# Performance work log

Hardware: AMD Instinct MI355X
Metric: run time of the kernel (lower is better)

Reference implementation:

```python
import jax, jax.numpy as jnp
import numpy as np

PAD_TOKEN = 1
V_EN = 32000
V_DE = 32000
WORD_DIM = 300
HID = 500
VLAYER = 500


def lstm(x, Wih, Whh, bih, bhh):
    """Single-layer batch-first LSTM, PyTorch gate order (i,f,g,o). x: [B,T,D] -> h: [B,T,H]."""
    xg = jnp.einsum('btd,gd->btg', x, Wih) + bih  # precompute input projections [B,T,4H]
    H = Whh.shape[1]
    B = x.shape[0]

    def step(carry, xg_t):
        h, c = carry
        g = xg_t + h @ Whh.T + bhh
        i, f, gg, o = jnp.split(g, 4, axis=-1)
        c = jax.nn.sigmoid(f) * c + jax.nn.sigmoid(i) * jnp.tanh(gg)
        h = jax.nn.sigmoid(o) * jnp.tanh(c)
        return (h, c), h

    h0 = jnp.zeros((B, H), x.dtype)
    (_, _), hs = jax.lax.scan(step, (h0, h0), jnp.swapaxes(xg, 0, 1))
    return jnp.swapaxes(hs, 0, 1)


def setup_inputs() -> dict:
    key = jax.random.key(0)
    ks = jax.random.split(key, 12)
    B, S, T = 64, 50, 50
    s = 0.05
    inp = {
        'x_de': jax.random.randint(ks[0], (B, S), 0, V_DE),
        'x_en': jax.random.randint(ks[1], (B, T), 0, V_EN),
        'emb_de_w': jax.random.normal(ks[2], (V_DE, WORD_DIM)) * s,
        'emb_en_w': jax.random.normal(ks[3], (V_EN, WORD_DIM)) * s,
        'enc_Wih': jax.random.normal(ks[4], (4 * HID, WORD_DIM)) * s,
        'enc_Whh': jax.random.normal(ks[5], (4 * HID, HID)) * s,
        'enc_bih': jnp.zeros((4 * HID,)),
        'enc_bhh': jnp.zeros((4 * HID,)),
        'dec_Wih': jax.random.normal(ks[6], (4 * HID, WORD_DIM)) * s,
        'dec_Whh': jax.random.normal(ks[7], (4 * HID, HID)) * s,
        'dec_bih': jnp.zeros((4 * HID,)),
        'dec_bhh': jnp.zeros((4 * HID,)),
        'h2e_w': jax.random.normal(ks[8], (VLAYER, 2 * HID)) * s,
        'h2e_b': jnp.zeros((VLAYER,)),
        'e2v_w': jax.random.normal(ks[9], (V_EN, VLAYER)) * s,
        'e2v_b': jnp.zeros((V_EN,)),
    }
    return inp


def reference(x_de, x_en, emb_de_w, emb_en_w,
              enc_Wih, enc_Whh, enc_bih, enc_bhh,
              dec_Wih, dec_Whh, dec_bih, dec_bhh,
              h2e_w, h2e_b, e2v_w, e2v_b):
    emb_de = emb_de_w[x_de]                       # [B,S,D]
    emb_en = emb_en_w[x_en]                       # [B,T,D]
    enc_h = lstm(emb_de, enc_Wih, enc_Whh, enc_bih, enc_bhh)  # [B,S,H]
    dec_h = lstm(emb_en, dec_Wih, dec_Whh, dec_bih, dec_bhh)  # [B,T,H]

    Tm1 = dec_h.shape[1] - 1
    scores = jnp.einsum('bsh,bth->bst', enc_h, dec_h[:, :Tm1])  # [B,S,T']

    # hard attention: categorical sample per (b,t), all timesteps vectorized
    logp_attn = jax.nn.log_softmax(scores, axis=1)               # [B,S,T']
    samples = jax.random.categorical(jax.random.key(42),
                                     jnp.swapaxes(scores, 1, 2), axis=-1)  # [B,T'] int
    context = jnp.take_along_axis(enc_h, samples[:, :, None], axis=1)      # [B,T',H]

    feat = jnp.concatenate([dec_h[:, :Tm1], context], axis=-1)   # [B,T',2H]
    e = jnp.tanh(feat @ h2e_w.T + h2e_b)
    pred = jax.nn.log_softmax(e @ e2v_w.T + e2v_b, axis=-1)      # [B,T',V]

    y = x_en[:, 1:]                                              # [B,T']
    mask = (y != PAD_TOKEN).astype(pred.dtype)
    reward = jnp.take_along_axis(pred, y[:, :, None], axis=-1)[..., 0]  # [B,T']
    cnt = jnp.maximum(mask.sum(0), 1.0)

    loss = -jnp.sum((reward * mask).sum(0) / cnt)

    logp_s = jnp.take_along_axis(jnp.swapaxes(logp_attn, 1, 2),
                                 samples[:, :, None], axis=-1)[..., 0]  # [B,T']
    baseline = jnp.log(1.0 / V_EN)
    adv = jax.lax.stop_gradient(reward - baseline)
    reinforce_loss = -jnp.sum((logp_s * adv * mask).sum(0) / cnt)

    return loss, reinforce_loss
```

## Files before the change

kernel.cpp:

```cpp
#include <hip/hip_runtime.h>
#include <cstdint>

typedef short short8 __attribute__((ext_vector_type(8)));
typedef float f32x4 __attribute__((ext_vector_type(4)));
typedef uint32_t u32x4 __attribute__((ext_vector_type(4)));
typedef unsigned short u16;
typedef unsigned long long u64;

__device__ __forceinline__ u16 f2bf(float f) {
  union { float f; uint32_t u; } v; v.f = f;
  uint32_t u = v.u;
  uint32_t r = (u + 0x7fffu + ((u >> 16) & 1u)) >> 16;
  return (u16)r;
}
__device__ __forceinline__ float bf2f(u16 b) {
  union { uint32_t u; float f; } v; v.u = ((uint32_t)b) << 16; return v.f;
}
__device__ __forceinline__ float sigm(float x) { return 1.f / (1.f + expf(-x)); }
__device__ __forceinline__ float tanh_f(float x) { return 2.f / (1.f + expf(-2.f * x)) - 1.f; }

typedef const __attribute__((address_space(1))) uint32_t glb_u32;
typedef __attribute__((address_space(3))) uint32_t lds_u32;
__device__ __forceinline__ void glds16(const void* g, void* l) {
  __builtin_amdgcn_global_load_lds((glb_u32*)g, (lds_u32*)l, 16, 0, 0);
}

__device__ __forceinline__ void tfround(uint32_t& a, uint32_t& b, int r) {
  a += b; b = (b << r) | (b >> (32 - r)); b ^= a;
}
__device__ __forceinline__ void threefry(uint32_t k0, uint32_t k1, uint32_t& x0, uint32_t& x1) {
  uint32_t k2 = k0 ^ k1 ^ 0x1BD11BDAu;
  x0 += k0; x1 += k1;
  tfround(x0,x1,13); tfround(x0,x1,15); tfround(x0,x1,26); tfround(x0,x1,6);
  x0 += k1; x1 += k2 + 1u;
  tfround(x0,x1,17); tfround(x0,x1,29); tfround(x0,x1,16); tfround(x0,x1,24);
  x0 += k2; x1 += k0 + 2u;
  tfround(x0,x1,13); tfround(x0,x1,15); tfround(x0,x1,26); tfround(x0,x1,6);
  x0 += k0; x1 += k1 + 3u;
  tfround(x0,x1,17); tfround(x0,x1,29); tfround(x0,x1,16); tfround(x0,x1,24);
  x0 += k1; x1 += k2 + 4u;
  tfround(x0,x1,13); tfround(x0,x1,15); tfround(x0,x1,26); tfround(x0,x1,6);
  x0 += k2; x1 += k0 + 5u;
}
__device__ __forceinline__ float gumbel_from_bits(uint32_t bits) {
  float f = __uint_as_float((bits >> 9) | 0x3f800000u) - 1.0f;
  const float tiny = 1.17549435e-38f;
  float u = fmaxf(f + tiny, tiny);
  return -logf(-logf(u));
}

__global__ __launch_bounds__(256) void prep_all(
    const float* eWih, const float* eWhh, const float* ebih, const float* ebhh,
    const float* dWih, const float* dWhh, const float* dbih, const float* dbhh,
    const float* h2e_w, const float* h2e_b, const float* e2v_w,
    u16* wih_p, u16* whh_p, float* bsum, u16* h2e_p, float* h2e_bp,
    u16* e2v_p, u16* hglob, int* bar)
{
  const uint32_t GWIH = 2u*2048u*40u;
  const uint32_t GWHH = 2u*2048u*64u;
  const uint32_t GBS  = 512u;
  const uint32_t GH2E = 512u*128u;
  const uint32_t GH2EB= 64u;
  const uint32_t GE2V = 32000u*64u;
  const uint32_t GHG  = 16384u;
  const uint32_t GBAR = 64u;
  const uint32_t TOT  = GWIH+GWHH+GBS+GH2E+GH2EB+GE2V+GHG+GBAR;
  for (uint32_t i = blockIdx.x*256u + threadIdx.x; i < TOT; i += gridDim.x*256u) {
    uint32_t j = i;
    if (j < GWIH) {
      uint32_t L = j / (2048u*40u), rem = j % (2048u*40u);
      uint32_t p = rem / 40u, kg = rem % 40u;
      uint32_t g = p >> 9, u = p & 511u, k0 = kg*8u;
      short8 o = {0,0,0,0,0,0,0,0}; u16* op = (u16*)&o;
      if (u < 500u) {
        const float* src = (L ? dWih : eWih) + ((size_t)(g*500u+u))*300u + k0;
        if (k0 + 8u <= 300u) {
          float4 a = *(const float4*)src, b = *(const float4*)(src+4);
          op[0]=f2bf(a.x);op[1]=f2bf(a.y);op[2]=f2bf(a.z);op[3]=f2bf(a.w);
          op[4]=f2bf(b.x);op[5]=f2bf(b.y);op[6]=f2bf(b.z);op[7]=f2bf(b.w);
        } else {
          #pragma unroll
          for (int e = 0; e < 8; ++e) if (k0+e < 300u) op[e] = f2bf(src[e]);
        }
      }
      *(short8*)(wih_p + (size_t)j*8) = o; continue;
    }
    j -= GWIH;
    if (j < GWHH) {
      uint32_t L = j / (2048u*64u), rem = j % (2048u*64u);
      uint32_t row = rem >> 6, kg = rem & 63u, k0 = kg*8u;
      uint32_t wg = row >> 7, r2 = row & 127u, g = r2 >> 5, ul = r2 & 31u;
      uint32_t u = wg*32u + ul;
      short8 o = {0,0,0,0,0,0,0,0}; u16* op = (u16*)&o;
      if (u < 500u) {
        const float* src = (L ? dWhh : eWhh) + ((size_t)(g*500u+u))*500u + k0;
        if (k0 + 8u <= 500u) {
          float4 a = *(const float4*)src, b = *(const float4*)(src+4);
          op[0]=f2bf(a.x);op[1]=f2bf(a.y);op[2]=f2bf(a.z);op[3]=f2bf(a.w);
          op[4]=f2bf(b.x);op[5]=f2bf(b.y);op[6]=f2bf(b.z);op[7]=f2bf(b.w);
        } else {
          #pragma unroll
          for (int e = 0; e < 8; ++e) if (k0+e < 500u) op[e] = f2bf(src[e]);
        }
      }
      *(short8*)(whh_p + (size_t)j*8) = o; continue;
    }
    j -= GWHH;
    if (j < GBS) {
      uint32_t L = j >> 8, pg = j & 255u, p0 = pg*8u;
      float arr[8];
      #pragma unroll
      for (int e = 0; e < 8; ++e) {
        uint32_t p = p0 + e, g = p >> 9, u = p & 511u;
        arr[e] = (u < 500u) ? ((L?dbih:ebih)[g*500u+u] + (L?dbhh:ebhh)[g*500u+u]) : 0.f;
      }
      *(float4*)(bsum + (size_t)j*8) = *(float4*)arr;
      *(float4*)(bsum + (size_t)j*8 + 4) = *(float4*)(arr+4);
      continue;
    }
    j -= GBS;
    if (j < GH2E) {
      uint32_t n = j >> 7, kg = j & 127u, k0 = kg*8u;
      short8 o = {0,0,0,0,0,0,0,0}; u16* op = (u16*)&o;
      if (n < 500u) {
        const float* rowp = h2e_w + (size_t)n*1000u;
        if (k0 + 8u <= 500u) {
          float4 a = *(const float4*)(rowp+k0), b = *(const float4*)(rowp+k0+4);
          op[0]=f2bf(a.x);op[1]=f2bf(a.y);op[2]=f2bf(a.z);op[3]=f2bf(a.w);
          op[4]=f2bf(b.x);op[5]=f2bf(b.y);op[6]=f2bf(b.z);op[7]=f2bf(b.w);
        } else if (k0 >= 512u && k0 + 8u <= 1012u) {
          #pragma unroll
          for (int e = 0; e < 8; ++e) op[e] = f2bf(rowp[k0 + e - 12u]);
        } else {
          #pragma unroll
          for (int e = 0; e < 8; ++e) {
            uint32_t k = k0 + e; float v = 0.f;
            if (k < 500u) v = rowp[k];
            else if (k >= 512u && k < 1012u) v = rowp[k - 12u];
            op[e] = f2bf(v);
          }
        }
      }
      *(short8*)(h2e_p + (size_t)j*8) = o; continue;
    }
    j -= GH2E;
    if (j < GH2EB) {
      uint32_t k0 = j*8u;
      float arr[8];
      #pragma unroll
      for (int e = 0; e < 8; ++e) { uint32_t k = k0+e; arr[e] = (k < 500u) ? h2e_b[k] : 0.f; }
      *(float4*)(h2e_bp + (size_t)j*8) = *(float4*)arr;
      *(float4*)(h2e_bp + (size_t)j*8 + 4) = *(float4*)(arr+4);
      continue;
    }
    j -= GH2EB;
    if (j < GE2V) {
      uint32_t n = j >> 6, kg = j & 63u, k0 = kg*8u;
      short8 o = {0,0,0,0,0,0,0,0}; u16* op = (u16*)&o;
      const float* src = e2v_w + (size_t)n*500u + k0;
      if (k0 + 8u <= 500u) {
        float4 a = *(const float4*)src, b = *(const float4*)(src+4);
        op[0]=f2bf(a.x);op[1]=f2bf(a.y);op[2]=f2bf(a.z);op[3]=f2bf(a.w);
        op[4]=f2bf(b.x);op[5]=f2bf(b.y);op[6]=f2bf(b.z);op[7]=f2bf(b.w);
      } else {
        #pragma unroll
        for (int e = 0; e < 8; ++e) if (k0+e < 500u) op[e] = f2bf(src[e]);
      }
      *(short8*)(e2v_p + (size_t)j*8) = o; continue;
    }
    j -= GE2V;
    if (j < GHG) { short8 z = {0,0,0,0,0,0,0,0}; *(short8*)(hglob + (size_t)j*8) = z; continue; }
    j -= GHG;
    if (j < GBAR) bar[j] = 0;
  }
}

__global__ __launch_bounds__(256, 1) void lstm_kernel(
    const u16* xg , const u16* whh_p,
    u16* hglob , float* h_out , int* bar)
{
  const int wg = blockIdx.x;
  const int lstm = wg >> 4;
  const int wgl = wg & 15;
  const int tid = threadIdx.x;
  const int wid = tid >> 6;
  const int lane = tid & 63;

  __shared__ u16 hbuf[64 * 512];
  __shared__ float pre[4][64][34];
  __shared__ u16 hsh[64 * 32];

  short8 wf[2][16];
  {
    const u16* wbase = whh_p + ((size_t)lstm*2048 + wgl*128 + wid*32) * 512;
    #pragma unroll
    for (int nt = 0; nt < 2; ++nt)
      #pragma unroll
      for (int kk = 0; kk < 16; ++kk) {
        int row = nt*16 + (lane & 15);
        int k = kk*32 + (lane >> 4)*8;
        wf[nt][kk] = *(const short8*)(wbase + (size_t)row*512 + k);
      }
  }

  float c[8];
  #pragma unroll
  for (int q = 0; q < 8; ++q) c[q] = 0.f;

  int* mybar = bar + lstm*32;
  const int ug = wgl*32 + (tid & 31);
  const u16* xgl = xg + ((size_t)lstm*3200)*2048;

  float xr[4][8];
  #pragma unroll
  for (int q = 0; q < 8; ++q) {
    int b = q*8 + (tid >> 5);
    size_t xrow = ((size_t)(b*50 + 0))*2048;
    #pragma unroll
    for (int g = 0; g < 4; ++g) xr[g][q] = bf2f(xgl[xrow + g*512 + ug]);
  }

  #pragma unroll 1
  for (int t = 0; t < 50; ++t) {
    const int cur = t & 1;
    {
      u32x4 sv[16];
      const char* sbase = (const char*)(hglob + ((size_t)(cur*2 + lstm))*64*512);
      #pragma unroll
      for (int i = 0; i < 16; ++i) {
        const void* p = sbase + (size_t)(i*256 + tid)*16;
        asm volatile("global_load_dwordx4 %0, %1, off sc0 sc1" : "=v"(sv[i]) : "v"(p));
      }
      asm volatile("s_waitcnt vmcnt(0)" ::: "memory");
      __builtin_amdgcn_sched_barrier(0);
      #pragma unroll
      for (int i = 0; i < 16; ++i) {
        int chunk = i*256 + tid;
        int row = chunk >> 6, col16 = chunk & 63;
        int byte = row*1024 + ((col16*16) ^ ((row & 7) << 4));
        *(u32x4*)((char*)hbuf + byte) = sv[i];
      }
    }
    __syncthreads();

    f32x4 zero = {0.f, 0.f, 0.f, 0.f};
    f32x4 acc[4][2];
    #pragma unroll
    for (int m = 0; m < 4; ++m) { acc[m][0] = zero; acc[m][1] = zero; }

    #pragma unroll
    for (int kk = 0; kk < 16; ++kk) {
      short8 af[4];
      #pragma unroll
      for (int m = 0; m < 4; ++m) {
        int row = m*16 + (lane & 15);
        int byte = row*1024 + ((kk*64 + (lane >> 4)*16) ^ ((row & 7) << 4));
        af[m] = *(const short8*)((const char*)hbuf + byte);
      }
      #pragma unroll
      for (int m = 0; m < 4; ++m) {
        acc[m][0] = __builtin_amdgcn_mfma_f32_16x16x32_bf16(af[m], wf[0][kk], acc[m][0], 0, 0, 0);
        acc[m][1] = __builtin_amdgcn_mfma_f32_16x16x32_bf16(af[m], wf[1][kk], acc[m][1], 0, 0, 0);
      }
    }

    #pragma unroll
    for (int m = 0; m < 4; ++m)
      #pragma unroll
      for (int nt = 0; nt < 2; ++nt)
        #pragma unroll
        for (int jj = 0; jj < 4; ++jj) {
          int row = m*16 + (lane >> 4)*4 + jj;
          int col = nt*16 + (lane & 15);
          pre[wid][row][col] = acc[m][nt][jj];
        }
    __syncthreads();

    #pragma unroll
    for (int q = 0; q < 8; ++q) {
      int b = q*8 + (tid >> 5);
      int ul = tid & 31;
      float pi = pre[0][b][ul] + xr[0][q];
      float pf = pre[1][b][ul] + xr[1][q];
      float pg = pre[2][b][ul] + xr[2][q];
      float po = pre[3][b][ul] + xr[3][q];
      c[q] = sigm(pf)*c[q] + sigm(pi)*tanh_f(pg);
      float h = sigm(po)*tanh_f(c[q]);
      if (ug >= 500) h = 0.f;
      h_out[(((size_t)(lstm*64 + b))*50 + t)*512 + ug] = h;
      hsh[b*32 + ul] = f2bf(h);
    }
    if (t == 49) break;
    __syncthreads();

    {
      u16* hdst = hglob + ((size_t)((cur^1)*2 + lstm))*64*512;
      int b2 = tid >> 2, c8 = (tid & 3)*8;
      u32x4 w = *(const u32x4*)(hsh + b2*32 + c8);
      void* dp = hdst + (size_t)b2*512 + wgl*32 + c8;
      asm volatile("global_store_dwordx4 %0, %1, off sc0 sc1" :: "v"(dp), "v"(w) : "memory");
    }
    asm volatile("s_waitcnt vmcnt(0)" ::: "memory");

    if (tid == 0)
      __hip_atomic_fetch_add(mybar, 1, __ATOMIC_RELAXED, __HIP_MEMORY_SCOPE_AGENT);

    {
      const int tn = t + 1;
      #pragma unroll
      for (int q = 0; q < 8; ++q) {
        int b = q*8 + (tid >> 5);
        size_t xrow = ((size_t)(b*50 + tn))*2048;
        #pragma unroll
        for (int g = 0; g < 4; ++g) xr[g][q] = bf2f(xgl[xrow + g*512 + ug]);
      }
    }

    if (tid == 0) {
      int target = 16*(t+1);
      while (__hip_atomic_load(mybar, __ATOMIC_RELAXED, __HIP_MEMORY_SCOPE_AGENT) < target) {}
    }
    __syncthreads();
  }
}

__global__ __launch_bounds__(256) void scores_kernel(const float* h_out, float* scores) {
  int b = blockIdx.x >> 2, tq = blockIdx.x & 3;
  int tid = threadIdx.x, wid = tid >> 6, lane = tid & 63;
  __shared__ float enc[50*512];
  const float* ebase = h_out + ((size_t)b*50)*512;
  for (int i = tid*4; i < 50*512; i += 256*4)
    *(float4*)(enc + i) = *(const float4*)(ebase + i);
  __syncthreads();
  const int t0 = tq*13;
  const int cnt = (tq == 3) ? 10 : 13;
  for (int tl = wid; tl < cnt; tl += 4) {
    int t = t0 + tl;
    const float* drow = h_out + ((size_t)((64 + b)*50 + t))*512;
    float d[8];
    #pragma unroll
    for (int j = 0; j < 8; ++j) d[j] = drow[lane + j*64];
    for (int s = 0; s < 50; ++s) {
      float p = 0.f;
      #pragma unroll
      for (int j = 0; j < 8; ++j) p += enc[s*512 + lane + j*64] * d[j];
      #pragma unroll
      for (int mk = 32; mk; mk >>= 1) p += __shfl_xor(p, mk);
      if (lane == 0) scores[((size_t)(b*50 + s))*49 + t] = p;
    }
  }
}

__global__ __launch_bounds__(256) void sample_kernel(const float* scores, int* samples, float* logp_s) {
  int p = blockIdx.x*4 + (threadIdx.x >> 6);
  int lane = threadIdx.x & 63;
  int b = p / 49, t = p - b*49;
  float sc = -INFINITY;
  if (lane < 50) sc = scores[((size_t)(b*50 + lane))*49 + t];
  float val = -INFINITY;
  if (lane < 50) {
    uint32_t i = (uint32_t)(p*50 + lane);
    uint32_t x0, x1; int sel;
    if (i < 78400u) { x0 = i; x1 = i + 78400u; sel = 0; }
    else            { x0 = i - 78400u; x1 = i; sel = 1; }
    threefry(0u, 42u, x0, x1);
    val = sc + gumbel_from_bits(sel ? x1 : x0);
  }
  int idx = lane; float v = val;
  #pragma unroll
  for (int mk = 1; mk < 64; mk <<= 1) {
    float ov = __shfl_xor(v, mk);
    int oi = __shfl_xor(idx, mk);
    if (ov > v || (ov == v && oi < idx)) { v = ov; idx = oi; }
  }
  float m = sc;
  #pragma unroll
  for (int mk = 1; mk < 64; mk <<= 1) m = fmaxf(m, __shfl_xor(m, mk));
  float e = (lane < 50) ? expf(sc - m) : 0.f;
  #pragma unroll
  for (int mk = 1; mk < 64; mk <<= 1) e += __shfl_xor(e, mk);
  float lse = m + logf(e);
  float scs = __shfl(sc, idx);
  if (lane == 0) { samples[p] = idx; logp_s[p] = scs - lse; }
}

template <int AMODE, int EPI>
__global__ __launch_bounds__(256) void gemm_k(
    const float* Af32a, const float* Af32b, const int* gia, const int* gib,
    const u16* Abf, const u16* Bp, int ldkB, int KT,
    float* Cf32, u16* Cbf, const float* bias,
    float* pm, float* ps, float* ylogit)
{
  int Mb, Nb;
  if constexpr (EPI == 2) {
    int bid = blockIdx.y*gridDim.x + blockIdx.x;
    const int NBLK = 25*250, q = NBLK/8, r = NBLK%8;
    int xcd = bid & 7, idx = bid >> 3;
    int wgid = (xcd < r ? xcd*(q+1) : r*(q+1) + (xcd-r)*q) + idx;
    Mb = wgid % 25; Nb = wgid / 25;
  } else { Mb = blockIdx.x; Nb = blockIdx.y; }
  const int zb = blockIdx.z;
  const int tid = threadIdx.x;
  const int wid = tid >> 6, lane = tid & 63;
  const int wr = wid >> 1, wc = wid & 1;

  __shared__ u16 As[2*128*64];
  __shared__ u16 Bs[2*128*64];
  __shared__ float part[128][2][2];

  f32x4 zero = {0.f,0.f,0.f,0.f};
  f32x4 acc[4][4];
  #pragma unroll
  for (int m = 0; m < 4; ++m)
    #pragma unroll
    for (int n = 0; n < 4; ++n) acc[m][n] = zero;

  auto MFMA_STEP = [&](int buf) {
    #pragma unroll
    for (int kk2 = 0; kk2 < 2; ++kk2) {
      short8 a[4], b[4];
      #pragma unroll
      for (int m = 0; m < 4; ++m) {
        int row = wr*64 + m*16 + (lane & 15);
        int byte = buf*16384 + row*128 + ((kk2*64 + (lane >> 4)*16) ^ ((row & 7) << 4));
        a[m] = *(const short8*)((const char*)As + byte);
      }
      #pragma unroll
      for (int n = 0; n < 4; ++n) {
        int row = wc*64 + n*16 + (lane & 15);
        int byte = buf*16384 + row*128 + ((kk2*64 + (lane >> 4)*16) ^ ((row & 7) << 4));
        b[n] = *(const short8*)((const char*)Bs + byte);
      }
      #pragma unroll
      for (int m = 0; m < 4; ++m)
        #pragma unroll
        for (int n = 0; n < 4; ++n)
          acc[m][n] = __builtin_amdgcn_mfma_f32_16x16x32_bf16(a[m], b[n], acc[m][n], 0, 0, 0);
    }
  };

  if constexpr (AMODE == 2) {
    auto ISSUE = [&](int it, int buf) {
      #pragma unroll
      for (int i = 0; i < 4; ++i) {
        int chunk = i*256 + tid;
        int row = chunk >> 3, c16 = chunk & 7;
        int cg = c16 ^ (row & 7);
        const u16* sa = Abf + (size_t)(Mb*128 + row)*512 + it*64 + cg*8;
        const u16* sb = Bp  + (size_t)(Nb*128 + row)*512 + it*64 + cg*8;
        char* da = (char*)As + buf*16384 + i*4096 + wid*1024;
        char* db = (char*)Bs + buf*16384 + i*4096 + wid*1024;
        glds16(sa, da);
        glds16(sb, db);
      }
    };
    ISSUE(0, 0);
    asm volatile("s_waitcnt vmcnt(0)" ::: "memory");
    __syncthreads();
    for (int it = 0; it < KT; ++it) {
      const int buf = it & 1;
      if (it + 1 < KT) ISSUE(it + 1, buf ^ 1);
      MFMA_STEP(buf);
      if (it + 1 < KT) {
        asm volatile("s_waitcnt vmcnt(0)" ::: "memory");
        __syncthreads();
      }
    }
  } else {
    const int r = tid >> 1;
    const int koff = (tid & 1)*32;
    const int growA = Mb*128 + r;
    const int growB = Nb*128 + r;

    const float* emb = nullptr; const int* ids = nullptr;
    int fb = 0, ft = 0, fsmp = 0; bool fvalid = true;
    if constexpr (AMODE == 0) {
      emb = zb ? Af32b : Af32a;
      ids = zb ? gib : gia;
    } else {
      fvalid = growA < 3136;
      fb = growA / 49; ft = growA - fb*49;
      fsmp = fvalid ? gia[growA] : 0;
    }

    short8 av8[4], bv8[4];
    auto FETCH = [&](int it) {
      const int k0 = it*64 + koff;
      u16* avp = (u16*)av8;
      if constexpr (AMODE == 0) {
        const float* srow = emb + (size_t)ids[growA]*300;
        #pragma unroll
        for (int j = 0; j < 8; ++j) {
          int k = k0 + j*4;
          float4 v = make_float4(0.f,0.f,0.f,0.f);
          if (k + 4 <= 300) v = *(const float4*)(srow + k);
          avp[j*4+0]=f2bf(v.x); avp[j*4+1]=f2bf(v.y); avp[j*4+2]=f2bf(v.z); avp[j*4+3]=f2bf(v.w);
        }
      } else {
        #pragma unroll
        for (int j = 0; j < 8; ++j) {
          int k = k0 + j*4;
          float4 v = make_float4(0.f,0.f,0.f,0.f);
          if (fvalid) {
            if (k + 4 <= 500) v = *(const float4*)(Af32a + ((size_t)(fb*50 + ft))*512 + k);
            else if (k >= 512 && k + 4 <= 1012) v = *(const float4*)(Af32b + ((size_t)(fb*50 + fsmp))*512 + (k - 512));
          }
          avp[j*4+0]=f2bf(v.x); avp[j*4+1]=f2bf(v.y); avp[j*4+2]=f2bf(v.z); avp[j*4+3]=f2bf(v.w);
        }
      }
      #pragma unroll
      for (int j = 0; j < 4; ++j)
        bv8[j] = *(const short8*)(Bp + (size_t)growB*ldkB + k0 + j*8);
    };
    auto STORE_LDS = [&](int buf) {
      #pragma unroll
      for (int j = 0; j < 4; ++j) {
        int byte = buf*16384 + r*128 + ((koff*2 + j*16) ^ ((r & 7) << 4));
        *(short8*)((char*)As + byte) = av8[j];
        *(short8*)((char*)Bs + byte) = bv8[j];
      }
    };

    FETCH(0);
    STORE_LDS(0);
    __syncthreads();
    for (int it = 0; it < KT; ++it) {
      const int cur = it & 1;
      if (it + 1 < KT) FETCH(it + 1);
      MFMA_STEP(cur);
      __syncthreads();
      if (it + 1 < KT) {
        STORE_LDS(cur ^ 1);
        __syncthreads();
      }
    }
  }

  if constexpr (EPI == 0) {
    u16* C = Cbf + (size_t)zb*3200*2048;
    const float* bs = bias + (size_t)zb*2048;
    #pragma unroll
    for (int m = 0; m < 4; ++m)
      #pragma unroll
      for (int n = 0; n < 4; ++n)
        #pragma unroll
        for (int jj = 0; jj < 4; ++jj) {
          int row = Mb*128 + wr*64 + m*16 + (lane >> 4)*4 + jj;
          int col = Nb*128 + wc*64 + n*16 + (lane & 15);
          C[(size_t)row*2048 + col] = f2bf(acc[m][n][jj] + bs[col]);
        }
  } else if constexpr (EPI == 1) {
    #pragma unroll
    for (int m = 0; m < 4; ++m)
      #pragma unroll
      for (int n = 0; n < 4; ++n)
        #pragma unroll
        for (int jj = 0; jj < 4; ++jj) {
          int row = Mb*128 + wr*64 + m*16 + (lane >> 4)*4 + jj;
          int col = Nb*128 + wc*64 + n*16 + (lane & 15);
          float e = tanh_f(acc[m][n][jj] + bias[col]);
          Cbf[(size_t)row*512 + col] = f2bf(e);
        }
  } else {
    float bias4[4];
    #pragma unroll
    for (int n = 0; n < 4; ++n) bias4[n] = bias[Nb*128 + wc*64 + n*16 + (lane & 15)];
    #pragma unroll
    for (int m = 0; m < 4; ++m)
      #pragma unroll
      for (int jj = 0; jj < 4; ++jj) {
        int trow = wr*64 + m*16 + (lane >> 4)*4 + jj;
        int grow = Mb*128 + trow;
        float x0 = acc[m][0][jj] + bias4[0];
        float x1 = acc[m][1][jj] + bias4[1];
        float x2 = acc[m][2][jj] + bias4[2];
        float x3 = acc[m][3][jj] + bias4[3];
        float mx = fmaxf(fmaxf(x0,x1), fmaxf(x2,x3));
        #pragma unroll
        for (int mk = 1; mk < 16; mk <<= 1) mx = fmaxf(mx, __shfl_xor(mx, mk));
        float sm = expf(x0-mx) + expf(x1-mx) + expf(x2-mx) + expf(x3-mx);
        #pragma unroll
        for (int mk = 1; mk < 16; mk <<= 1) sm += __shfl_xor(sm, mk);
        if (grow < 3136) {
          int b = grow / 49, tt = grow - b*49;
          int yv = gib[b*50 + tt + 1];
          int cb = yv - (Nb*128 + wc*64);
          if (cb == 0*16 + (lane & 15)) ylogit[grow] = x0;
          if (cb == 1*16 + (lane & 15)) ylogit[grow] = x1;
          if (cb == 2*16 + (lane & 15)) ylogit[grow] = x2;
          if (cb == 3*16 + (lane & 15)) ylogit[grow] = x3;
        }
        if ((lane & 15) == 0) { part[trow][wc][0] = mx; part[trow][wc][1] = sm; }
      }
    __syncthreads();
    if (tid < 128) {
      int grow = Mb*128 + tid;
      if (grow < 3136) {
        float m0 = part[tid][0][0], s0 = part[tid][0][1];
        float m1 = part[tid][1][0], s1 = part[tid][1][1];
        float M = fmaxf(m0, m1);
        float S = s0*expf(m0 - M) + s1*expf(m1 - M);
        pm[(size_t)grow*250 + Nb] = M;
        ps[(size_t)grow*250 + Nb] = S;
      }
    }
  }
}

__global__ __launch_bounds__(256) void lse_reduce(const float* pm, const float* ps,
                                                  const float* ylogit, float* reward) {
  int row = blockIdx.x*4 + (threadIdx.x >> 6);
  int lane = threadIdx.x & 63;
  if (row >= 3136) return;
  float M = -INFINITY, S = 0.f;
  for (int j = lane; j < 250; j += 64) {
    float m = pm[(size_t)row*250 + j], s = ps[(size_t)row*250 + j];
    float nm = fmaxf(M, m);
    S = S*expf(M - nm) + s*expf(m - nm);
    M = nm;
  }
  #pragma unroll
  for (int mk = 1; mk < 64; mk <<= 1) {
    float om = __shfl_xor(M, mk), os = __shfl_xor(S, mk);
    float nm = fmaxf(M, om);
    S = S*expf(M - nm) + os*expf(om - nm);
    M = nm;
  }
  if (lane == 0) reward[row] = ylogit[row] - (M + logf(S));
}

__global__ void final_kernel(const float* reward, const float* logp_s, const int* x_en, float* out) {
  int t = threadIdx.x;
  float tl = 0.f, trl = 0.f;
  const float baseline = logf(1.0f / 32000.0f);
  if (t < 49) {
    float sr = 0.f, srl = 0.f; int cm = 0;
    for (int b = 0; b < 64; ++b) {
      int yv = x_en[b*50 + t + 1];
      if (yv != 1) {
        float rw = reward[b*49 + t];
        sr += rw;
        srl += logp_s[b*49 + t] * (rw - baseline);
        cm += 1;
      }
    }
    float cnt = fmaxf((float)cm, 1.f);
    tl = sr / cnt; trl = srl / cnt;
  }
  #pragma unroll
  for (int mk = 1; mk < 64; mk <<= 1) { tl += __shfl_xor(tl, mk); trl += __shfl_xor(trl, mk); }
  if (t == 0) { out[0] = -tl; out[1] = -trl; }
}

extern "C" void kernel_launch(void* const* d_in, const int* in_sizes, int n_in,
                              void* d_out, int out_size, void* d_ws, size_t ws_size,
                              hipStream_t stream) {
  (void)in_sizes; (void)n_in; (void)out_size; (void)ws_size;
  const int*   x_de    = (const int*)d_in[0];
  const int*   x_en    = (const int*)d_in[1];
  const float* emb_de  = (const float*)d_in[2];
  const float* emb_en  = (const float*)d_in[3];
  const float* enc_Wih = (const float*)d_in[4];
  const float* enc_Whh = (const float*)d_in[5];
  const float* enc_bih = (const float*)d_in[6];
  const float* enc_bhh = (const float*)d_in[7];
  const float* dec_Wih = (const float*)d_in[8];
  const float* dec_Whh = (const float*)d_in[9];
  const float* dec_bih = (const float*)d_in[10];
  const float* dec_bhh = (const float*)d_in[11];
  const float* h2e_w   = (const float*)d_in[12];
  const float* h2e_b   = (const float*)d_in[13];
  const float* e2v_w   = (const float*)d_in[14];
  const float* e2v_b   = (const float*)d_in[15];
  float* out = (float*)d_out;

  char* ws = (char*)d_ws;
  size_t o = 0;
  auto alloc = [&](size_t bytes) { size_t rr = o; o += (bytes + 255) & ~(size_t)255; return rr; };
  int*   bar     = (int*)  (ws + alloc(256));
  u16*   wih_p   = (u16*)  (ws + alloc(2ull*2048*320*2));
  u16*   whh_p   = (u16*)  (ws + alloc(2ull*2048*512*2));
  float* bsum    = (float*)(ws + alloc(2ull*2048*4));
  u16*   h2e_p   = (u16*)  (ws + alloc(512ull*1024*2));
  float* h2e_bp  = (float*)(ws + alloc(512ull*4));
  u16*   e2v_p   = (u16*)  (ws + alloc(32000ull*512*2));
  u16*   xg      = (u16*)  (ws + alloc(2ull*3200*2048*2));
  u16*   hglob   = (u16*)  (ws + alloc(2ull*2*64*512*2));
  float* h_out   = (float*)(ws + alloc(2ull*64*50*512*4));
  float* scores  = (float*)(ws + alloc(64ull*50*49*4));
  int*   samples = (int*)  (ws + alloc(3136ull*4));
  float* logp_s  = (float*)(ws + alloc(3136ull*4));
  float* ylogit  = (float*)(ws + alloc(3200ull*4));
  float* reward  = (float*)(ws + alloc(3136ull*4));
  u16*   e_buf   = (u16*)  (ws + alloc(3200ull*512*2));
  float* pmb     = (float*)(ws + alloc(3200ull*250*4));
  float* psb     = (float*)(ws + alloc(3200ull*250*4));

  prep_all<<<2048, 256, 0, stream>>>(enc_Wih, enc_Whh, enc_bih, enc_bhh,
      dec_Wih, dec_Whh, dec_bih, dec_bhh, h2e_w, h2e_b, e2v_w,
      wih_p, whh_p, bsum, h2e_p, h2e_bp, e2v_p, hglob, bar);

  gemm_k<0,0><<<dim3(25,16,2), 256, 0, stream>>>(emb_de, emb_en, x_de, x_en,
      nullptr, wih_p, 320, 5, nullptr, xg, bsum, nullptr, nullptr, nullptr);

  lstm_kernel<<<32, 256, 0, stream>>>(xg, whh_p, hglob, h_out, bar);

  scores_kernel<<<256, 256, 0, stream>>>(h_out, scores);

  sample_kernel<<<784, 256, 0, stream>>>(scores, samples, logp_s);

  gemm_k<1,1><<<dim3(25,4,1), 256, 0, stream>>>(h_out + 64ull*50*512, h_out, samples, nullptr,
      nullptr, h2e_p, 1024, 16, nullptr, e_buf, h2e_bp, nullptr, nullptr, nullptr);

  gemm_k<2,2><<<dim3(25,250,1), 256, 0, stream>>>(nullptr, nullptr, nullptr, x_en,
      e_buf, e2v_p, 512, 8, nullptr, nullptr, e2v_b, pmb, psb, ylogit);

  lse_reduce<<<784, 256, 0, stream>>>(pmb, psb, ylogit, reward);

  final_kernel<<<1, 64, 0, stream>>>(reward, logp_s, x_en, out);
}
```

Before: 815.6 us.

## Overlap output-weight conversion with LSTM recurrence and split h loads into halves

```diff
diff --git a/kernel.cpp b/kernel.cpp
--- a/kernel.cpp
+++ b/kernel.cpp
@@ -49,22 +49,17 @@
   return -logf(-logf(u));
 }
 
-__global__ __launch_bounds__(256) void prep_all(
+__global__ __launch_bounds__(256) void prep_lstm(
     const float* eWih, const float* eWhh, const float* ebih, const float* ebhh,
     const float* dWih, const float* dWhh, const float* dbih, const float* dbhh,
-    const float* h2e_w, const float* h2e_b, const float* e2v_w,
-    u16* wih_p, u16* whh_p, float* bsum, u16* h2e_p, float* h2e_bp,
-    u16* e2v_p, u16* hglob, int* bar)
+    u16* wih_p, u16* whh_p, float* bsum, u16* hglob, int* bar)
 {
   const uint32_t GWIH = 2u*2048u*40u;
   const uint32_t GWHH = 2u*2048u*64u;
   const uint32_t GBS  = 512u;
-  const uint32_t GH2E = 512u*128u;
-  const uint32_t GH2EB= 64u;
-  const uint32_t GE2V = 32000u*64u;
   const uint32_t GHG  = 16384u;
   const uint32_t GBAR = 64u;
-  const uint32_t TOT  = GWIH+GWHH+GBS+GH2E+GH2EB+GE2V+GHG+GBAR;
+  const uint32_t TOT  = GWIH+GWHH+GBS+GHG+GBAR;
   for (uint32_t i = blockIdx.x*256u + threadIdx.x; i < TOT; i += gridDim.x*256u) {
     uint32_t j = i;
     if (j < GWIH) {
@@ -119,76 +114,91 @@
       continue;
     }
     j -= GBS;
-    if (j < GH2E) {
-      uint32_t n = j >> 7, kg = j & 127u, k0 = kg*8u;
-      short8 o = {0,0,0,0,0,0,0,0}; u16* op = (u16*)&o;
-      if (n < 500u) {
-        const float* rowp = h2e_w + (size_t)n*1000u;
-        if (k0 + 8u <= 500u) {
-          float4 a = *(const float4*)(rowp+k0), b = *(const float4*)(rowp+k0+4);
-          op[0]=f2bf(a.x);op[1]=f2bf(a.y);op[2]=f2bf(a.z);op[3]=f2bf(a.w);
-          op[4]=f2bf(b.x);op[5]=f2bf(b.y);op[6]=f2bf(b.z);op[7]=f2bf(b.w);
-        } else if (k0 >= 512u && k0 + 8u <= 1012u) {
-          #pragma unroll
-          for (int e = 0; e < 8; ++e) op[e] = f2bf(rowp[k0 + e - 12u]);
-        } else {
-          #pragma unroll
-          for (int e = 0; e < 8; ++e) {
-            uint32_t k = k0 + e; float v = 0.f;
-            if (k < 500u) v = rowp[k];
-            else if (k >= 512u && k < 1012u) v = rowp[k - 12u];
-            op[e] = f2bf(v);
-          }
-        }
-      }
-      *(short8*)(h2e_p + (size_t)j*8) = o; continue;
-    }
-    j -= GH2E;
-    if (j < GH2EB) {
-      uint32_t k0 = j*8u;
-      float arr[8];
-      #pragma unroll
-      for (int e = 0; e < 8; ++e) { uint32_t k = k0+e; arr[e] = (k < 500u) ? h2e_b[k] : 0.f; }
-      *(float4*)(h2e_bp + (size_t)j*8) = *(float4*)arr;
-      *(float4*)(h2e_bp + (size_t)j*8 + 4) = *(float4*)(arr+4);
-      continue;
-    }
-    j -= GH2EB;
-    if (j < GE2V) {
-      uint32_t n = j >> 6, kg = j & 63u, k0 = kg*8u;
-      short8 o = {0,0,0,0,0,0,0,0}; u16* op = (u16*)&o;
-      const float* src = e2v_w + (size_t)n*500u + k0;
-      if (k0 + 8u <= 500u) {
-        float4 a = *(const float4*)src, b = *(const float4*)(src+4);
-        op[0]=f2bf(a.x);op[1]=f2bf(a.y);op[2]=f2bf(a.z);op[3]=f2bf(a.w);
-        op[4]=f2bf(b.x);op[5]=f2bf(b.y);op[6]=f2bf(b.z);op[7]=f2bf(b.w);
-      } else {
-        #pragma unroll
-        for (int e = 0; e < 8; ++e) if (k0+e < 500u) op[e] = f2bf(src[e]);
-      }
-      *(short8*)(e2v_p + (size_t)j*8) = o; continue;
-    }
-    j -= GE2V;
     if (j < GHG) { short8 z = {0,0,0,0,0,0,0,0}; *(short8*)(hglob + (size_t)j*8) = z; continue; }
     j -= GHG;
     if (j < GBAR) bar[j] = 0;
   }
 }
 
-__global__ __launch_bounds__(256, 1) void lstm_kernel(
+__global__ __launch_bounds__(256, 1) void lstm_fused(
     const u16* xg , const u16* whh_p,
-    u16* hglob , float* h_out , int* bar)
+    u16* hglob , float* h_out , int* bar,
+    const float* h2e_w, const float* h2e_b, const float* e2v_w,
+    u16* h2e_p, float* h2e_bp, u16* e2v_p)
 {
+  const int tid = threadIdx.x;
+
+  if (blockIdx.x >= 32) {
+    const uint32_t GH2E = 512u*128u;
+    const uint32_t GH2EB= 64u;
+    const uint32_t GE2V = 32000u*64u;
+    const uint32_t TOT  = GH2E + GH2EB + GE2V;
+    const uint32_t stride = (gridDim.x - 32u)*256u;
+    for (uint32_t i = (blockIdx.x - 32u)*256u + tid; i < TOT; i += stride) {
+      uint32_t j = i;
+      if (j < GH2E) {
+        uint32_t n = j >> 7, kg = j & 127u, k0 = kg*8u;
+        short8 o = {0,0,0,0,0,0,0,0}; u16* op = (u16*)&o;
+        if (n < 500u) {
+          const float* rowp = h2e_w + (size_t)n*1000u;
+          if (k0 + 8u <= 500u) {
+            float4 a = *(const float4*)(rowp+k0), b = *(const float4*)(rowp+k0+4);
+            op[0]=f2bf(a.x);op[1]=f2bf(a.y);op[2]=f2bf(a.z);op[3]=f2bf(a.w);
+            op[4]=f2bf(b.x);op[5]=f2bf(b.y);op[6]=f2bf(b.z);op[7]=f2bf(b.w);
+          } else if (k0 >= 512u && k0 + 8u <= 1012u) {
+            #pragma unroll
+            for (int e = 0; e < 8; ++e) op[e] = f2bf(rowp[k0 + e - 12u]);
+          } else {
+            #pragma unroll
+            for (int e = 0; e < 8; ++e) {
+              uint32_t k = k0 + e; float v = 0.f;
+              if (k < 500u) v = rowp[k];
+              else if (k >= 512u && k < 1012u) v = rowp[k - 12u];
+              op[e] = f2bf(v);
+            }
+          }
+        }
+        *(short8*)(h2e_p + (size_t)j*8) = o; continue;
+      }
+      j -= GH2E;
+      if (j < GH2EB) {
+        uint32_t k0 = j*8u;
+        float arr[8];
+        #pragma unroll
+        for (int e = 0; e < 8; ++e) { uint32_t k = k0+e; arr[e] = (k < 500u) ? h2e_b[k] : 0.f; }
+        *(float4*)(h2e_bp + (size_t)j*8) = *(float4*)arr;
+        *(float4*)(h2e_bp + (size_t)j*8 + 4) = *(float4*)(arr+4);
+        continue;
+      }
+      j -= GH2EB;
+      {
+        uint32_t n = j >> 6, kg = j & 63u, k0 = kg*8u;
+        short8 o = {0,0,0,0,0,0,0,0}; u16* op = (u16*)&o;
+        const float* src = e2v_w + (size_t)n*500u + k0;
+        if (k0 + 8u <= 500u) {
+          float4 a = *(const float4*)src, b = *(const float4*)(src+4);
+          op[0]=f2bf(a.x);op[1]=f2bf(a.y);op[2]=f2bf(a.z);op[3]=f2bf(a.w);
+          op[4]=f2bf(b.x);op[5]=f2bf(b.y);op[6]=f2bf(b.z);op[7]=f2bf(b.w);
+        } else {
+          #pragma unroll
+          for (int e = 0; e < 8; ++e) if (k0+e < 500u) op[e] = f2bf(src[e]);
+        }
+        *(short8*)(e2v_p + (size_t)j*8) = o;
+      }
+    }
+    return;
+  }
+
   const int wg = blockIdx.x;
   const int lstm = wg >> 4;
   const int wgl = wg & 15;
-  const int tid = threadIdx.x;
   const int wid = tid >> 6;
   const int lane = tid & 63;
 
   __shared__ u16 hbuf[64 * 512];
   __shared__ float pre[4][64][34];
   __shared__ u16 hsh[64 * 32];
+  __shared__ u16 xsh[4 * 64 * 32];
 
   short8 wf[2][16];
   {
@@ -211,87 +221,144 @@
   const int ug = wgl*32 + (tid & 31);
   const u16* xgl = xg + ((size_t)lstm*3200)*2048;
 
-  float xr[4][8];
-  #pragma unroll
-  for (int q = 0; q < 8; ++q) {
-    int b = q*8 + (tid >> 5);
-    size_t xrow = ((size_t)(b*50 + 0))*2048;
-    #pragma unroll
-    for (int g = 0; g < 4; ++g) xr[g][q] = bf2f(xgl[xrow + g*512 + ug]);
+  {
+    #pragma unroll
+    for (int jj = 0; jj < 4; ++jj) {
+      int chunk = jj*256 + tid;
+      int g = chunk >> 8, b = (chunk >> 2) & 63, u8 = chunk & 3;
+      short8 v = *(const short8*)(xgl + (size_t)(b*50 + 0)*2048 + g*512 + wgl*32 + u8*8);
+      *(short8*)(xsh + chunk*8) = v;
+    }
   }
 
   #pragma unroll 1
   for (int t = 0; t < 50; ++t) {
     const int cur = t & 1;
     {
+      asm volatile("s_waitcnt vmcnt(0)" ::: "memory");
       u32x4 sv[16];
       const char* sbase = (const char*)(hglob + ((size_t)(cur*2 + lstm))*64*512);
       #pragma unroll
-      for (int i = 0; i < 16; ++i) {
-        const void* p = sbase + (size_t)(i*256 + tid)*16;
+      for (int i = 0; i < 8; ++i) {
+        int cchunk = i*256 + tid;
+        int row = cchunk >> 5, col16 = cchunk & 31;
+        const void* p = sbase + (size_t)row*1024 + col16*16;
         asm volatile("global_load_dwordx4 %0, %1, off sc0 sc1" : "=v"(sv[i]) : "v"(p));
       }
+      #pragma unroll
+      for (int i = 0; i < 8; ++i) {
+        int cchunk = i*256 + tid;
+        int row = cchunk >> 5, col16 = 32 + (cchunk & 31);
+        const void* p = sbase + (size_t)row*1024 + col16*16;
+        asm volatile("global_load_dwordx4 %0, %1, off sc0 sc1" : "=v"(sv[8+i]) : "v"(p));
+      }
+      asm volatile("s_waitcnt vmcnt(8)" ::: "memory");
+      __builtin_amdgcn_sched_barrier(0);
+      #pragma unroll
+      for (int i = 0; i < 8; ++i) {
+        int cchunk = i*256 + tid;
+        int row = cchunk >> 5, col16 = cchunk & 31;
+        int byte = row*1024 + ((col16*16) ^ ((row & 7) << 4));
+        *(u32x4*)((char*)hbuf + byte) = sv[i];
+      }
+      __syncthreads();
+
+      f32x4 zero = {0.f, 0.f, 0.f, 0.f};
+      f32x4 acc[4][2];
+      #pragma unroll
+      for (int m = 0; m < 4; ++m) { acc[m][0] = zero; acc[m][1] = zero; }
+
+      #pragma unroll
+      for (int kk = 0; kk < 8; ++kk) {
+        short8 af[4];
+        #pragma unroll
+        for (int m = 0; m < 4; ++m) {
+          int row = m*16 + (lane & 15);
+          int byte = row*1024 + ((kk*64 + (lane >> 4)*16) ^ ((row & 7) << 4));
+          af[m] = *(const short8*)((const char*)hbuf + byte);
+        }
+        #pragma unroll
+        for (int m = 0; m < 4; ++m) {
+          acc[m][0] = __builtin_amdgcn_mfma_f32_16x16x32_bf16(af[m], wf[0][kk], acc[m][0], 0, 0, 0);
+          acc[m][1] = __builtin_amdgcn_mfma_f32_16x16x32_bf16(af[m], wf[1][kk], acc[m][1], 0, 0, 0);
+        }
+      }
+
       asm volatile("s_waitcnt vmcnt(0)" ::: "memory");
       __builtin_amdgcn_sched_barrier(0);
       #pragma unroll
-      for (int i = 0; i < 16; ++i) {
-        int chunk = i*256 + tid;
-        int row = chunk >> 6, col16 = chunk & 63;
+      for (int i = 0; i < 8; ++i) {
+        int cchunk = i*256 + tid;
+        int row = cchunk >> 5, col16 = 32 + (cchunk & 31);
         int byte = row*1024 + ((col16*16) ^ ((row & 7) << 4));
-        *(u32x4*)((char*)hbuf + byte) = sv[i];
-      }
+        *(u32x4*)((char*)hbuf + byte) = sv[8+i];
+      }
+      __syncthreads();
+
+      #pragma unroll
+      for (int kk = 8; kk < 16; ++kk) {
+        short8 af[4];
+        #pragma unroll
+        for (int m = 0; m < 4; ++m) {
+          int row = m*16 + (lane & 15);
+          int byte = row*1024 + ((kk*64 + (lane >> 4)*16) ^ ((row & 7) << 4));
+          af[m] = *(const short8*)((const char*)hbuf + byte);
+        }
+        #pragma unroll
+        for (int m = 0; m < 4; ++m) {
+          acc[m][0] = __builtin_amdgcn_mfma_f32_16x16x32_bf16(af[m], wf[0][kk], acc[m][0], 0, 0, 0);
+          acc[m][1] = __builtin_amdgcn_mfma_f32_16x16x32_bf16(af[m], wf[1][kk], acc[m][1], 0, 0, 0);
+        }
+      }
+
+      #pragma unroll
+      for (int m = 0; m < 4; ++m)
+        #pragma unroll
+        for (int nt = 0; nt < 2; ++nt)
+          #pragma unroll
+          for (int jj = 0; jj < 4; ++jj) {
+            int row = m*16 + (lane >> 4)*4 + jj;
+            int col = nt*16 + (lane & 15);
+            pre[wid][row][col] = acc[m][nt][jj];
+          }
     }
     __syncthreads();
 
-    f32x4 zero = {0.f, 0.f, 0.f, 0.f};
-    f32x4 acc[4][2];
-    #pragma unroll
-    for (int m = 0; m < 4; ++m) { acc[m][0] = zero; acc[m][1] = zero; }
-
-    #pragma unroll
-    for (int kk = 0; kk < 16; ++kk) {
-      short8 af[4];
-      #pragma unroll
-      for (int m = 0; m < 4; ++m) {
-        int row = m*16 + (lane & 15);
-        int byte = row*1024 + ((kk*64 + (lane >> 4)*16) ^ ((row & 7) << 4));
-        af[m] = *(const short8*)((const char*)hbuf + byte);
-      }
-      #pragma unroll
-      for (int m = 0; m < 4; ++m) {
-        acc[m][0] = __builtin_amdgcn_mfma_f32_16x16x32_bf16(af[m], wf[0][kk], acc[m][0], 0, 0, 0);
-        acc[m][1] = __builtin_amdgcn_mfma_f32_16x16x32_bf16(af[m], wf[1][kk], acc[m][1], 0, 0, 0);
-      }
-    }
-
-    #pragma unroll
-    for (int m = 0; m < 4; ++m)
-      #pragma unroll
-      for (int nt = 0; nt < 2; ++nt)
-        #pragma unroll
-        for (int jj = 0; jj < 4; ++jj) {
-          int row = m*16 + (lane >> 4)*4 + jj;
-          int col = nt*16 + (lane & 15);
-          pre[wid][row][col] = acc[m][nt][jj];
-        }
-    __syncthreads();
-
+    float hq[8];
     #pragma unroll
     for (int q = 0; q < 8; ++q) {
       int b = q*8 + (tid >> 5);
       int ul = tid & 31;
-      float pi = pre[0][b][ul] + xr[0][q];
-      float pf = pre[1][b][ul] + xr[1][q];
-      float pg = pre[2][b][ul] + xr[2][q];
-      float po = pre[3][b][ul] + xr[3][q];
+      float pi = pre[0][b][ul] + bf2f(xsh[(0*64 + b)*32 + ul]);
+      float pf = pre[1][b][ul] + bf2f(xsh[(1*64 + b)*32 + ul]);
+      float pg = pre[2][b][ul] + bf2f(xsh[(2*64 + b)*32 + ul]);
+      float po = pre[3][b][ul] + bf2f(xsh[(3*64 + b)*32 + ul]);
       c[q] = sigm(pf)*c[q] + sigm(pi)*tanh_f(pg);
       float h = sigm(po)*tanh_f(c[q]);
       if (ug >= 500) h = 0.f;
-      h_out[(((size_t)(lstm*64 + b))*50 + t)*512 + ug] = h;
+      hq[q] = h;
       hsh[b*32 + ul] = f2bf(h);
     }
-    if (t == 49) break;
+    if (t == 49) {
+      #pragma unroll
+      for (int q = 0; q < 8; ++q) {
+        int b = q*8 + (tid >> 5);
+        h_out[(((size_t)(lstm*64 + b))*50 + t)*512 + ug] = hq[q];
+      }
+      break;
+    }
     __syncthreads();
+
+    short8 xv[4];
+    {
+      const int tn = t + 1;
+      #pragma unroll
+      for (int jj = 0; jj < 4; ++jj) {
+        int chunk = jj*256 + tid;
+        int g = chunk >> 8, b = (chunk >> 2) & 63, u8 = chunk & 3;
+        xv[jj] = *(const short8*)(xgl + (size_t)(b*50 + tn)*2048 + g*512 + wgl*32 + u8*8);
+      }
+    }
 
     {
       u16* hdst = hglob + ((size_t)((cur^1)*2 + lstm))*64*512;
@@ -305,15 +372,13 @@
     if (tid == 0)
       __hip_atomic_fetch_add(mybar, 1, __ATOMIC_RELAXED, __HIP_MEMORY_SCOPE_AGENT);
 
-    {
-      const int tn = t + 1;
-      #pragma unroll
-      for (int q = 0; q < 8; ++q) {
-        int b = q*8 + (tid >> 5);
-        size_t xrow = ((size_t)(b*50 + tn))*2048;
-        #pragma unroll
-        for (int g = 0; g < 4; ++g) xr[g][q] = bf2f(xgl[xrow + g*512 + ug]);
-      }
+    #pragma unroll
+    for (int jj = 0; jj < 4; ++jj)
+      *(short8*)(xsh + (jj*256 + tid)*8) = xv[jj];
+    #pragma unroll
+    for (int q = 0; q < 8; ++q) {
+      int b = q*8 + (tid >> 5);
+      h_out[(((size_t)(lstm*64 + b))*50 + t)*512 + ug] = hq[q];
     }
 
     if (tid == 0) {
@@ -696,14 +761,14 @@
   float* pmb     = (float*)(ws + alloc(3200ull*250*4));
   float* psb     = (float*)(ws + alloc(3200ull*250*4));
 
-  prep_all<<<2048, 256, 0, stream>>>(enc_Wih, enc_Whh, enc_bih, enc_bhh,
-      dec_Wih, dec_Whh, dec_bih, dec_bhh, h2e_w, h2e_b, e2v_w,
-      wih_p, whh_p, bsum, h2e_p, h2e_bp, e2v_p, hglob, bar);
+  prep_lstm<<<512, 256, 0, stream>>>(enc_Wih, enc_Whh, enc_bih, enc_bhh,
+      dec_Wih, dec_Whh, dec_bih, dec_bhh, wih_p, whh_p, bsum, hglob, bar);
 
   gemm_k<0,0><<<dim3(25,16,2), 256, 0, stream>>>(emb_de, emb_en, x_de, x_en,
       nullptr, wih_p, 320, 5, nullptr, xg, bsum, nullptr, nullptr, nullptr);
 
-  lstm_kernel<<<32, 256, 0, stream>>>(xg, whh_p, hglob, h_out, bar);
+  lstm_fused<<<1024, 256, 0, stream>>>(xg, whh_p, hglob, h_out, bar,
+      h2e_w, h2e_b, e2v_w, h2e_p, h2e_bp, e2v_p);
 
   scores_kernel<<<256, 256, 0, stream>>>(h_out, scores);
 
```

Result: no change. 831.7 us (+2.0%).

## Move h2e/e2v weight conversion into extra z-slice of input-projection GEMM

Applied to the files above, without the earlier changes.

```diff
diff --git a/kernel.cpp b/kernel.cpp
--- a/kernel.cpp
+++ b/kernel.cpp
@@ -49,22 +49,17 @@
   return -logf(-logf(u));
 }
 
-__global__ __launch_bounds__(256) void prep_all(
+__global__ __launch_bounds__(256) void prep_lstm(
     const float* eWih, const float* eWhh, const float* ebih, const float* ebhh,
     const float* dWih, const float* dWhh, const float* dbih, const float* dbhh,
-    const float* h2e_w, const float* h2e_b, const float* e2v_w,
-    u16* wih_p, u16* whh_p, float* bsum, u16* h2e_p, float* h2e_bp,
-    u16* e2v_p, u16* hglob, int* bar)
+    u16* wih_p, u16* whh_p, float* bsum, u16* hglob, int* bar)
 {
   const uint32_t GWIH = 2u*2048u*40u;
   const uint32_t GWHH = 2u*2048u*64u;
   const uint32_t GBS  = 512u;
-  const uint32_t GH2E = 512u*128u;
-  const uint32_t GH2EB= 64u;
-  const uint32_t GE2V = 32000u*64u;
   const uint32_t GHG  = 16384u;
   const uint32_t GBAR = 64u;
-  const uint32_t TOT  = GWIH+GWHH+GBS+GH2E+GH2EB+GE2V+GHG+GBAR;
+  const uint32_t TOT  = GWIH+GWHH+GBS+GHG+GBAR;
   for (uint32_t i = blockIdx.x*256u + threadIdx.x; i < TOT; i += gridDim.x*256u) {
     uint32_t j = i;
     if (j < GWIH) {
@@ -119,56 +114,6 @@
       continue;
     }
     j -= GBS;
-    if (j < GH2E) {
-      uint32_t n = j >> 7, kg = j & 127u, k0 = kg*8u;
-      short8 o = {0,0,0,0,0,0,0,0}; u16* op = (u16*)&o;
-      if (n < 500u) {
-        const float* rowp = h2e_w + (size_t)n*1000u;
-        if (k0 + 8u <= 500u) {
-          float4 a = *(const float4*)(rowp+k0), b = *(const float4*)(rowp+k0+4);
-          op[0]=f2bf(a.x);op[1]=f2bf(a.y);op[2]=f2bf(a.z);op[3]=f2bf(a.w);
-          op[4]=f2bf(b.x);op[5]=f2bf(b.y);op[6]=f2bf(b.z);op[7]=f2bf(b.w);
-        } else if (k0 >= 512u && k0 + 8u <= 1012u) {
-          #pragma unroll
-          for (int e = 0; e < 8; ++e) op[e] = f2bf(rowp[k0 + e - 12u]);
-        } else {
-          #pragma unroll
-          for (int e = 0; e < 8; ++e) {
-            uint32_t k = k0 + e; float v = 0.f;
-            if (k < 500u) v = rowp[k];
-            else if (k >= 512u && k < 1012u) v = rowp[k - 12u];
-            op[e] = f2bf(v);
-          }
-        }
-      }
-      *(short8*)(h2e_p + (size_t)j*8) = o; continue;
-    }
-    j -= GH2E;
-    if (j < GH2EB) {
-      uint32_t k0 = j*8u;
-      float arr[8];
-      #pragma unroll
-      for (int e = 0; e < 8; ++e) { uint32_t k = k0+e; arr[e] = (k < 500u) ? h2e_b[k] : 0.f; }
-      *(float4*)(h2e_bp + (size_t)j*8) = *(float4*)arr;
-      *(float4*)(h2e_bp + (size_t)j*8 + 4) = *(float4*)(arr+4);
-      continue;
-    }
-    j -= GH2EB;
-    if (j < GE2V) {
-      uint32_t n = j >> 6, kg = j & 63u, k0 = kg*8u;
-      short8 o = {0,0,0,0,0,0,0,0}; u16* op = (u16*)&o;
-      const float* src = e2v_w + (size_t)n*500u + k0;
-      if (k0 + 8u <= 500u) {
-        float4 a = *(const float4*)src, b = *(const float4*)(src+4);
-        op[0]=f2bf(a.x);op[1]=f2bf(a.y);op[2]=f2bf(a.z);op[3]=f2bf(a.w);
-        op[4]=f2bf(b.x);op[5]=f2bf(b.y);op[6]=f2bf(b.z);op[7]=f2bf(b.w);
-      } else {
-        #pragma unroll
-        for (int e = 0; e < 8; ++e) if (k0+e < 500u) op[e] = f2bf(src[e]);
-      }
-      *(short8*)(e2v_p + (size_t)j*8) = o; continue;
-    }
-    j -= GE2V;
     if (j < GHG) { short8 z = {0,0,0,0,0,0,0,0}; *(short8*)(hglob + (size_t)j*8) = z; continue; }
     j -= GHG;
     if (j < GBAR) bar[j] = 0;
@@ -389,8 +334,78 @@
     const float* Af32a, const float* Af32b, const int* gia, const int* gib,
     const u16* Abf, const u16* Bp, int ldkB, int KT,
     float* Cf32, u16* Cbf, const float* bias,
-    float* pm, float* ps, float* ylogit)
+    float* pm, float* ps, float* ylogit,
+    const float* pr_h2e_w = nullptr, const float* pr_h2e_b = nullptr,
+    const float* pr_e2v_w = nullptr, u16* pr_h2e_p = nullptr,
+    float* pr_h2e_bp = nullptr, u16* pr_e2v_p = nullptr)
 {
+  const int zb = blockIdx.z;
+  const int tid = threadIdx.x;
+
+  if constexpr (AMODE == 0) {
+    if (zb == 2) {
+      const uint32_t GH2E = 512u*128u;
+      const uint32_t GH2EB= 64u;
+      const uint32_t GE2V = 32000u*64u;
+      const uint32_t TOT  = GH2E + GH2EB + GE2V;
+      const uint32_t pid  = blockIdx.y*gridDim.x + blockIdx.x;
+      const uint32_t stride = gridDim.x*gridDim.y*256u;
+      for (uint32_t i = pid*256u + tid; i < TOT; i += stride) {
+        uint32_t j = i;
+        if (j < GH2E) {
+          uint32_t n = j >> 7, kg = j & 127u, k0 = kg*8u;
+          short8 o = {0,0,0,0,0,0,0,0}; u16* op = (u16*)&o;
+          if (n < 500u) {
+            const float* rowp = pr_h2e_w + (size_t)n*1000u;
+            if (k0 + 8u <= 500u) {
+              float4 a = *(const float4*)(rowp+k0), b = *(const float4*)(rowp+k0+4);
+              op[0]=f2bf(a.x);op[1]=f2bf(a.y);op[2]=f2bf(a.z);op[3]=f2bf(a.w);
+              op[4]=f2bf(b.x);op[5]=f2bf(b.y);op[6]=f2bf(b.z);op[7]=f2bf(b.w);
+            } else if (k0 >= 512u && k0 + 8u <= 1012u) {
+              #pragma unroll
+              for (int e = 0; e < 8; ++e) op[e] = f2bf(rowp[k0 + e - 12u]);
+            } else {
+              #pragma unroll
+              for (int e = 0; e < 8; ++e) {
+                uint32_t k = k0 + e; float v = 0.f;
+                if (k < 500u) v = rowp[k];
+                else if (k >= 512u && k < 1012u) v = rowp[k - 12u];
+                op[e] = f2bf(v);
+              }
+            }
+          }
+          *(short8*)(pr_h2e_p + (size_t)j*8) = o; continue;
+        }
+        j -= GH2E;
+        if (j < GH2EB) {
+          uint32_t k0 = j*8u;
+          float arr[8];
+          #pragma unroll
+          for (int e = 0; e < 8; ++e) { uint32_t k = k0+e; arr[e] = (k < 500u) ? pr_h2e_b[k] : 0.f; }
+          *(float4*)(pr_h2e_bp + (size_t)j*8) = *(float4*)arr;
+          *(float4*)(pr_h2e_bp + (size_t)j*8 + 4) = *(float4*)(arr+4);
+          continue;
+        }
+        j -= GH2EB;
+        {
+          uint32_t n = j >> 6, kg = j & 63u, k0 = kg*8u;
+          short8 o = {0,0,0,0,0,0,0,0}; u16* op = (u16*)&o;
+          const float* src = pr_e2v_w + (size_t)n*500u + k0;
+          if (k0 + 8u <= 500u) {
+            float4 a = *(const float4*)src, b = *(const float4*)(src+4);
+            op[0]=f2bf(a.x);op[1]=f2bf(a.y);op[2]=f2bf(a.z);op[3]=f2bf(a.w);
+            op[4]=f2bf(b.x);op[5]=f2bf(b.y);op[6]=f2bf(b.z);op[7]=f2bf(b.w);
+          } else {
+            #pragma unroll
+            for (int e = 0; e < 8; ++e) if (k0+e < 500u) op[e] = f2bf(src[e]);
+          }
+          *(short8*)(pr_e2v_p + (size_t)j*8) = o;
+        }
+      }
+      return;
+    }
+  }
+
   int Mb, Nb;
   if constexpr (EPI == 2) {
     int bid = blockIdx.y*gridDim.x + blockIdx.x;
@@ -399,8 +414,6 @@
     int wgid = (xcd < r ? xcd*(q+1) : r*(q+1) + (xcd-r)*q) + idx;
     Mb = wgid % 25; Nb = wgid / 25;
   } else { Mb = blockIdx.x; Nb = blockIdx.y; }
-  const int zb = blockIdx.z;
-  const int tid = threadIdx.x;
   const int wid = tid >> 6, lane = tid & 63;
   const int wr = wid >> 1, wc = wid & 1;
 
@@ -696,12 +709,12 @@
   float* pmb     = (float*)(ws + alloc(3200ull*250*4));
   float* psb     = (float*)(ws + alloc(3200ull*250*4));
 
-  prep_all<<<2048, 256, 0, stream>>>(enc_Wih, enc_Whh, enc_bih, enc_bhh,
-      dec_Wih, dec_Whh, dec_bih, dec_bhh, h2e_w, h2e_b, e2v_w,
-      wih_p, whh_p, bsum, h2e_p, h2e_bp, e2v_p, hglob, bar);
-
-  gemm_k<0,0><<<dim3(25,16,2), 256, 0, stream>>>(emb_de, emb_en, x_de, x_en,
-      nullptr, wih_p, 320, 5, nullptr, xg, bsum, nullptr, nullptr, nullptr);
+  prep_lstm<<<512, 256, 0, stream>>>(enc_Wih, enc_Whh, enc_bih, enc_bhh,
+      dec_Wih, dec_Whh, dec_bih, dec_bhh, wih_p, whh_p, bsum, hglob, bar);
+
+  gemm_k<0,0><<<dim3(25,16,3), 256, 0, stream>>>(emb_de, emb_en, x_de, x_en,
+      nullptr, wih_p, 320, 5, nullptr, xg, bsum, nullptr, nullptr, nullptr,
+      h2e_w, h2e_b, e2v_w, h2e_p, h2e_bp, e2v_p);
 
   lstm_kernel<<<32, 256, 0, stream>>>(xg, whh_p, hglob, h_out, bar);
 
```

Measured after the change: 820.4 us. No clear change (+0.6%).
